# Kernel tuning notes

Measured on AMD Instinct MI355X. Metric: run time of the kernel, lower is better.

## Reference

```python
import jax, jax.numpy as jnp
import numpy as np

RADIUS = 0.1
NSAMPLE = 32


def setup_inputs() -> dict:
    key = jax.random.key(0)
    k1, k2, k3, k4, k5 = jax.random.split(key, 5)
    B, NPOINT, N, C = 4, 2048, 8192, 64
    query_xyz = jax.random.uniform(k1, (B, 3, NPOINT), dtype=jnp.float32)
    support_xyz = jax.random.uniform(k2, (B, 3, N), dtype=jnp.float32)
    query_mask = jax.random.bernoulli(k3, 0.9, (B, NPOINT))
    support_mask = jax.random.bernoulli(k4, 0.9, (B, N))
    features = jax.random.normal(k5, (B, C, N), dtype=jnp.float32)
    return {"query_xyz": query_xyz, "support_xyz": support_xyz,
            "query_mask": query_mask, "support_mask": support_mask,
            "features": features}


def _masked_ordered_ball_query(query_xyz, support_xyz, query_mask, support_mask,
                               radius, nsample):
    # query_xyz: (B,3,npoint), support_xyz: (B,3,N)
    q = query_xyz.transpose(0, 2, 1)    # (B, npoint, 3)
    s = support_xyz.transpose(0, 2, 1)  # (B, N, 3)
    N = s.shape[1]
    # squared pairwise distances via |q|^2 + |s|^2 - 2 q.s  -> (B, npoint, N)
    d2 = (jnp.sum(q * q, -1)[:, :, None]
          + jnp.sum(s * s, -1)[:, None, :]
          - 2.0 * jnp.einsum('bpd,bnd->bpn', q, s))
    within = (d2 <= radius * radius) \
        & support_mask[:, None, :] & query_mask[:, :, None]
    # ordered selection of the first `nsample` in-ball indices (ascending index)
    score = jnp.where(within, N - jnp.arange(N, dtype=jnp.int32), 0)
    vals, idx = jax.lax.top_k(score, nsample)     # (B, npoint, nsample)
    idx_mask = vals > 0                            # true neighbors
    # pad slots with the first found neighbor (0 if none found)
    first = jnp.where(idx_mask[..., :1], idx[..., :1], 0)
    idx = jnp.where(idx_mask, idx, first)
    return idx, idx_mask


def _group(points_nc, idx):
    # points_nc: (B, N, D), idx: (B, npoint, nsample) -> (B, npoint, nsample, D)
    return jax.vmap(lambda p, i: p[i])(points_nc, idx)


def reference(query_xyz, support_xyz, query_mask, support_mask, features):
    idx, idx_mask = _masked_ordered_ball_query(
        query_xyz, support_xyz, query_mask, support_mask, RADIUS, NSAMPLE)
    s = support_xyz.transpose(0, 2, 1)             # (B, N, 3)
    grouped_xyz = _group(s, idx).transpose(0, 3, 1, 2)   # (B,3,npoint,nsample)
    grouped_xyz = grouped_xyz - query_xyz[:, :, :, None]
    grouped_xyz = grouped_xyz / RADIUS             # normalize_xyz=True
    f = features.transpose(0, 2, 1)                # (B, N, C)
    grouped_features = _group(f, idx).transpose(0, 3, 1, 2)  # (B,C,npoint,nsample)
    new_features = jnp.concatenate([grouped_xyz, grouped_features], axis=1)
    return new_features, idx_mask
```

## Files before the change

### kernel.cpp

```cpp
#include <hip/hip_runtime.h>


#define NPOINT 2048
#define NSUP   8192
#define NCH    64
#define NS     32
#define GRID1  10
#define CELLS  1000
#define QCHUNK 1024

__device__ __forceinline__ bool probe_mask4(const void* mask) {
    const unsigned char* mb = (const unsigned char*)mask;
    const int lane = threadIdx.x & 63;
    return __ballot(mb[4 * lane + 1] != 0) == 0ull;
}
__device__ __forceinline__ bool read_mask(const void* mask, int i, bool is4) {
    return is4 ? (((const int*)mask)[i] != 0)
               : (((const unsigned char*)mask)[i] != 0);
}
__device__ __forceinline__ int cell_of(float x, float y, float z) {
    const int cx = min(GRID1 - 1, (int)(x * 10.0f));
    const int cy = min(GRID1 - 1, (int)(y * 10.0f));
    const int cz = min(GRID1 - 1, (int)(z * 10.0f));
    return cx + GRID1 * cy + GRID1 * GRID1 * cz;
}

__global__ __launch_bounds__(256) void zero_ws(int* __restrict__ ptr, int n) {
    const int i = blockIdx.x * 256 + threadIdx.x;
    if (i < n) ptr[i] = 0;
}

__global__ __launch_bounds__(256) void grid_hist(
    const float* __restrict__ support_xyz, const void* __restrict__ support_mask,
    int* __restrict__ starts)
{
    const bool m4 = probe_mask4(support_mask);
    const int gid = blockIdx.x * 256 + threadIdx.x;
    const int b = gid / NSUP, n = gid % NSUP;
    if (!read_mask(support_mask, gid, m4)) return;
    const float* sx = support_xyz + (size_t)b * 3 * NSUP;
    const int cid = cell_of(sx[n], sx[NSUP + n], sx[2 * NSUP + n]);
    atomicAdd(&starts[b * (CELLS + 1) + cid + 1], 1);
}

__global__ __launch_bounds__(1024) void grid_scan(int* __restrict__ starts) {
    __shared__ int scanb[1024];
    const int tid = threadIdx.x;
    int* sb = starts + blockIdx.x * (CELLS + 1);
    scanb[tid] = (tid < CELLS) ? sb[tid + 1] : 0;
    __syncthreads();
    for (int d = 1; d < 1024; d <<= 1) {
        int v = 0;
        if (tid >= d) v = scanb[tid - d];
        __syncthreads();
        if (tid >= d) scanb[tid] += v;
        __syncthreads();
    }
    if (tid < CELLS) sb[tid + 1] = scanb[tid];
}

__global__ __launch_bounds__(256) void grid_fill(
    const float* __restrict__ support_xyz, const void* __restrict__ support_mask,
    const int* __restrict__ starts, int* __restrict__ cursors,
    float4* __restrict__ pts)
{
    const bool m4 = probe_mask4(support_mask);
    const int gid = blockIdx.x * 256 + threadIdx.x;
    const int b = gid / NSUP, n = gid % NSUP;
    if (!read_mask(support_mask, gid, m4)) return;
    const float* sx = support_xyz + (size_t)b * 3 * NSUP;
    const float x = sx[n], y = sx[NSUP + n], z = sx[2 * NSUP + n];
    const int cid = cell_of(x, y, z);
    const int pos = starts[b * (CELLS + 1) + cid]
                  + atomicAdd(&cursors[b * CELLS + cid], 1);
    pts[(size_t)b * NSUP + pos] = make_float4(x, y, z, __int_as_float(n));
}

__global__ __launch_bounds__(256) void mqag_query(
    const float* __restrict__ query_xyz, const float* __restrict__ support_xyz,
    const void* __restrict__ query_mask, const void* __restrict__ support_mask,
    const float4* __restrict__ pts, const int* __restrict__ starts,
    int* __restrict__ idx_ws, float* __restrict__ out, int B)
{
#pragma clang fp contract(off)
    const int wib  = threadIdx.x >> 6;
    const int lane = threadIdx.x & 63;
    const int qid  = blockIdx.x * 4 + wib;
    const int b    = qid / NPOINT;
    const int p    = qid % NPOINT;

    __shared__ int hits_all[4][64];
    __shared__ int slots_all[4][NS];
    int* hits  = hits_all[wib];
    int* slots = slots_all[wib];

    const bool m4s = probe_mask4(support_mask);
    const bool m4q = probe_mask4(query_mask);

    const float* sx = support_xyz + (size_t)b * 3 * NSUP;
    const float* sy = sx + NSUP;
    const float* sz = sx + 2 * NSUP;

    const float qx = query_xyz[(size_t)b * 3 * NPOINT + p];
    const float qy = query_xyz[(size_t)b * 3 * NPOINT + NPOINT + p];
    const float qz = query_xyz[(size_t)b * 3 * NPOINT + 2 * NPOINT + p];
    const bool  qm = read_mask(query_mask, b * NPOINT + p, m4q);
    const float qq = (qx * qx + qy * qy) + qz * qz;

    int cnt = 0;
    if (qm) {
        const int x0 = max(0, (int)floorf((qx - 0.101f) * 10.f));
        const int x1 = min(GRID1 - 1, (int)floorf((qx + 0.101f) * 10.f));
        const int y0 = max(0, (int)floorf((qy - 0.101f) * 10.f));
        const int y1 = min(GRID1 - 1, (int)floorf((qy + 0.101f) * 10.f));
        const int z0 = max(0, (int)floorf((qz - 0.101f) * 10.f));
        const int z1 = min(GRID1 - 1, (int)floorf((qz + 0.101f) * 10.f));
        const int ncx = x1 - x0 + 1;

        const int*    stb  = starts + b * (CELLS + 1);
        const float4* ptsb = pts + (size_t)b * NSUP;

        for (int cz = z0; cz <= z1; ++cz) {
            for (int cy = y0; cy <= y1; ++cy) {
                const int c0 = x0 + GRID1 * cy + GRID1 * GRID1 * cz;
                const int s0 = stb[c0];
                const int e0 = stb[c0 + ncx];
                for (int tb = s0; tb < e0; tb += 64) {
                    const int g  = tb + lane;
                    const bool valid = g < e0;
                    const float4 pv = ptsb[valid ? g : (e0 - 1)];
                    const int nidx = __float_as_int(pv.w);
                    const float ss  = (pv.x * pv.x + pv.y * pv.y) + pv.z * pv.z;
                    const float dot = __builtin_fmaf(qz, pv.z,
                                      __builtin_fmaf(qy, pv.y, qx * pv.x));
                    const float d2  = (qq + ss) - 2.0f * dot;
                    const bool within = valid && (d2 <= 0.01f)
                        && read_mask(support_mask, b * NSUP + nidx, m4s);
                    const unsigned long long bal = __ballot(within);
                    if (within) {
                        const int r = cnt + __popcll(bal & ((1ull << lane) - 1ull));
                        if (r < 64) hits[r] = nidx;
                    }
                    cnt += __popcll(bal);
                }
            }
        }
    }

    __syncthreads();

    if (cnt > 64) {
        int c2 = 0;
        for (int basei = 0; basei < NSUP; basei += 64) {
            const int n = basei + lane;
            const float x = sx[n], y = sy[n], z = sz[n];
            const bool  m = read_mask(support_mask, b * NSUP + n, m4s);
            const float ss  = (x * x + y * y) + z * z;
            const float dot = __builtin_fmaf(qz, z,
                              __builtin_fmaf(qy, y, qx * x));
            const float d2  = (qq + ss) - 2.0f * dot;
            const bool within = (d2 <= 0.01f) && m;
            const unsigned long long bal = __ballot(within);
            if (within) {
                const int r = c2 + __popcll(bal & ((1ull << lane) - 1ull));
                if (r < NS) slots[r] = n;
            }
            c2 += __popcll(bal);
            if (c2 >= NS) break;
        }
        cnt = c2;
    } else {
        int v = (lane < cnt) ? hits[lane] : 0x7FFFFFFF;
        #pragma unroll
        for (int k = 2; k <= 64; k <<= 1) {
            #pragma unroll
            for (int j = k >> 1; j > 0; j >>= 1) {
                const int pv = __shfl_xor(v, j, 64);
                const bool keep_min = ((lane & j) == 0) == ((lane & k) == 0);
                const int mn = min(v, pv), mx = max(v, pv);
                v = keep_min ? mn : mx;
            }
        }
        if (lane < NS && lane < cnt) slots[lane] = v;
    }
    const int found = (cnt < NS) ? cnt : NS;

    __syncthreads();
    const int first = (found > 0) ? slots[0] : 0;
    if (lane < NS && lane >= found) slots[lane] = first;
    __syncthreads();

    if (lane < NS) idx_ws[((size_t)b * NPOINT + p) * NS + lane] = slots[lane];

    const size_t nf_elems = (size_t)B * 67 * NPOINT * NS;
    if (lane < NS) {
        out[nf_elems + ((size_t)b * NPOINT + p) * NS + lane] =
            (lane < found) ? 1.0f : 0.0f;
    }

    for (int i = 0; i < 2; ++i) {
        const int flat = i * 64 + lane;
        if (flat < 3 * NS) {
            const int ch = flat >> 5;
            const int k  = flat & 31;
            const int idx = slots[k];
            const float s = sx[(size_t)ch * NSUP + idx];
            const float q = (ch == 0) ? qx : ((ch == 1) ? qy : qz);
            out[(((size_t)b * 67 + ch) * NPOINT + p) * NS + k] = (s - q) / 0.1f;
        }
    }
}

__global__ __launch_bounds__(256) void gather_feat(
    const float* __restrict__ features, const int* __restrict__ idx_ws,
    float* __restrict__ out, int B)
{
    __shared__ float row[NSUP];
    const int bc = blockIdx.y;
    const int b  = bc / NCH, ch = bc % NCH;
    const int p0 = blockIdx.x * QCHUNK;

    const float* src = features + ((size_t)b * NCH + ch) * NSUP;
    const float4* src4 = (const float4*)src;
    for (int i = threadIdx.x; i < NSUP / 4; i += 256)
        ((float4*)row)[i] = src4[i];
    __syncthreads();

    const int4* idx4 = (const int4*)(idx_ws + ((size_t)b * NPOINT + p0) * NS);
    float4* dst4 = (float4*)(out + (((size_t)b * 67 + 3 + ch) * NPOINT + p0) * NS);
    for (int e = threadIdx.x; e < QCHUNK * NS / 4; e += 256) {
        const int4 iv = idx4[e];
        dst4[e] = make_float4(row[iv.x], row[iv.y], row[iv.z], row[iv.w]);
    }
}

__global__ __launch_bounds__(256) void mqag_linear(
    const float* __restrict__ query_xyz, const float* __restrict__ support_xyz,
    const void* __restrict__ query_mask_raw, const void* __restrict__ support_mask_raw,
    const float* __restrict__ features, float* __restrict__ out, int B)
{
#pragma clang fp contract(off)
    const int wib  = threadIdx.x >> 6;
    const int lane = threadIdx.x & 63;
    const int qid  = blockIdx.x * 4 + wib;
    const int b    = qid / NPOINT;
    const int p    = qid % NPOINT;

    __shared__ int slots_all[4][NS];
    int* slots = slots_all[wib];

    const bool m4s = probe_mask4(support_mask_raw);
    const bool m4q = probe_mask4(query_mask_raw);

    const float* sx = support_xyz + (size_t)b * 3 * NSUP;
    const float* sy = sx + NSUP;
    const float* sz = sx + 2 * NSUP;

    const float qx = query_xyz[(size_t)b * 3 * NPOINT + p];
    const float qy = query_xyz[(size_t)b * 3 * NPOINT + NPOINT + p];
    const float qz = query_xyz[(size_t)b * 3 * NPOINT + 2 * NPOINT + p];
    const bool  qm = read_mask(query_mask_raw, b * NPOINT + p, m4q);
    const float qq = (qx * qx + qy * qy) + qz * qz;

    int cnt = 0;
    if (qm) {
        for (int base = 0; base < NSUP; base += 64) {
            const int n = base + lane;
            const float x = sx[n], y = sy[n], z = sz[n];
            const bool  m = read_mask(support_mask_raw, b * NSUP + n, m4s);
            const float ss  = (x * x + y * y) + z * z;
            const float dot = __builtin_fmaf(qz, z, __builtin_fmaf(qy, y, qx * x));
            const float d2  = (qq + ss) - 2.0f * dot;
            const bool within = (d2 <= 0.01f) && m;
            const unsigned long long bal = __ballot(within);
            if (within) {
                const int r = cnt + __popcll(bal & ((1ull << lane) - 1ull));
                if (r < NS) slots[r] = n;
            }
            cnt += __popcll(bal);
            if (cnt >= NS) break;
        }
    }
    const int found = cnt < NS ? cnt : NS;
    __syncthreads();
    const int first = (found > 0) ? slots[0] : 0;
    if (lane < NS && lane >= found) slots[lane] = first;
    __syncthreads();

    const size_t nf_elems = (size_t)B * 67 * NPOINT * NS;
    if (lane < NS) {
        out[nf_elems + ((size_t)b * NPOINT + p) * NS + lane] =
            (lane < found) ? 1.0f : 0.0f;
    }
    const float* feat = features + (size_t)b * NCH * NSUP;
    for (int i = 0; i < (67 * NS + 63) / 64; ++i) {
        const int flat = i * 64 + lane;
        if (flat < 67 * NS) {
            const int ch = flat >> 5;
            const int k  = flat & 31;
            const int idx = slots[k];
            float val;
            if (ch < 3) {
                const float s = sx[(size_t)ch * NSUP + idx];
                const float q = (ch == 0) ? qx : ((ch == 1) ? qy : qz);
                val = (s - q) / 0.1f;
            } else {
                val = feat[(size_t)(ch - 3) * NSUP + idx];
            }
            out[(((size_t)b * 67 + ch) * NPOINT + p) * NS + k] = val;
        }
    }
}

extern "C" void kernel_launch(void* const* d_in, const int* in_sizes, int n_in,
                              void* d_out, int out_size, void* d_ws, size_t ws_size,
                              hipStream_t stream) {
    const float* query_xyz    = (const float*)d_in[0];
    const float* support_xyz  = (const float*)d_in[1];
    const void*  query_mask   = d_in[2];
    const void*  support_mask = d_in[3];
    const float* features     = (const float*)d_in[4];

    const int B = in_sizes[0] / (3 * NPOINT);

    const size_t off_pts     = 0;
    const size_t off_starts  = off_pts + (size_t)B * NSUP * sizeof(float4);
    const size_t off_cursors = off_starts + (size_t)B * (CELLS + 1) * sizeof(int);
    const size_t off_idx     = off_cursors + (size_t)B * CELLS * sizeof(int);
    const size_t need = off_idx + (size_t)B * NPOINT * NS * sizeof(int);

    if (ws_size >= need) {
        float4* pts  = (float4*)((char*)d_ws + off_pts);
        int* starts  = (int*)((char*)d_ws + off_starts);
        int* cursors = (int*)((char*)d_ws + off_cursors);
        int* idx_ws  = (int*)((char*)d_ws + off_idx);

        const int nzero = B * (CELLS + 1) + B * CELLS;
        hipLaunchKernelGGL(zero_ws, dim3((nzero + 255) / 256), dim3(256), 0,
                           stream, starts, nzero);
        hipLaunchKernelGGL(grid_hist, dim3(B * NSUP / 256), dim3(256), 0,
                           stream, support_xyz, support_mask, starts);
        hipLaunchKernelGGL(grid_scan, dim3(B), dim3(1024), 0, stream, starts);
        hipLaunchKernelGGL(grid_fill, dim3(B * NSUP / 256), dim3(256), 0,
                           stream, support_xyz, support_mask, starts, cursors, pts);
        hipLaunchKernelGGL(mqag_query, dim3(B * NPOINT / 4), dim3(256), 0,
                           stream, query_xyz, support_xyz, query_mask,
                           support_mask, pts, starts, idx_ws, (float*)d_out, B);
        hipLaunchKernelGGL(gather_feat, dim3(NPOINT / QCHUNK, B * NCH), dim3(256),
                           0, stream, features, idx_ws, (float*)d_out, B);
    } else {
        hipLaunchKernelGGL(mqag_linear, dim3(B * NPOINT / 4), dim3(256), 0,
                           stream, query_xyz, support_xyz, query_mask,
                           support_mask, features, (float*)d_out, B);
    }
}
```

Before: 123.3 us.

## Fuse grid build into one per-batch kernel and flatten cell-row scan loop

The four grid-construction kernels (zero, histogram, scan, fill) become a single per-batch block that builds the histogram and cursors in shared memory. This removes three launches and the global atomics. The query kernel now prefix-sums the cell-row lengths across lanes and walks all candidate rows as one flat range, so partially filled 64-wide iterations at each row boundary go away. It also drops the redundant support-mask check, since masked points are never inserted into the grid. In exchange, grid build runs on only B blocks, which leaves most of the device idle and serialises that phase.

New measurement: 116.6 us. 1.06x faster.

```diff
diff --git a/kernel.cpp b/kernel.cpp
--- a/kernel.cpp
+++ b/kernel.cpp
@@ -25,29 +25,35 @@
     return cx + GRID1 * cy + GRID1 * GRID1 * cz;
 }
 
-__global__ __launch_bounds__(256) void zero_ws(int* __restrict__ ptr, int n) {
-    const int i = blockIdx.x * 256 + threadIdx.x;
-    if (i < n) ptr[i] = 0;
-}
-
-__global__ __launch_bounds__(256) void grid_hist(
+__global__ __launch_bounds__(1024) void build_grid(
     const float* __restrict__ support_xyz, const void* __restrict__ support_mask,
-    int* __restrict__ starts)
+    int* __restrict__ starts, float4* __restrict__ pts)
 {
+    __shared__ int hist[CELLS];
+    __shared__ int scanb[1024];
+    __shared__ int cur[CELLS];
+    const int b   = blockIdx.x;
+    const int tid = threadIdx.x;
     const bool m4 = probe_mask4(support_mask);
-    const int gid = blockIdx.x * 256 + threadIdx.x;
-    const int b = gid / NSUP, n = gid % NSUP;
-    if (!read_mask(support_mask, gid, m4)) return;
     const float* sx = support_xyz + (size_t)b * 3 * NSUP;
-    const int cid = cell_of(sx[n], sx[NSUP + n], sx[2 * NSUP + n]);
-    atomicAdd(&starts[b * (CELLS + 1) + cid + 1], 1);
-}
-
-__global__ __launch_bounds__(1024) void grid_scan(int* __restrict__ starts) {
-    __shared__ int scanb[1024];
-    const int tid = threadIdx.x;
-    int* sb = starts + blockIdx.x * (CELLS + 1);
-    scanb[tid] = (tid < CELLS) ? sb[tid + 1] : 0;
+
+    if (tid < CELLS) { hist[tid] = 0; cur[tid] = 0; }
+    __syncthreads();
+
+    float xr[8], yr[8], zr[8]; int cidr[8]; bool mr[8];
+    #pragma unroll
+    for (int i = 0; i < 8; ++i) {
+        const int n = tid + 1024 * i;
+        xr[i] = sx[n];
+        yr[i] = sx[NSUP + n];
+        zr[i] = sx[2 * NSUP + n];
+        mr[i] = read_mask(support_mask, b * NSUP + n, m4);
+        cidr[i] = cell_of(xr[i], yr[i], zr[i]);
+        if (mr[i]) atomicAdd(&hist[cidr[i]], 1);
+    }
+    __syncthreads();
+
+    scanb[tid] = (tid < CELLS) ? hist[tid] : 0;
     __syncthreads();
     for (int d = 1; d < 1024; d <<= 1) {
         int v = 0;
@@ -56,24 +62,20 @@
         if (tid >= d) scanb[tid] += v;
         __syncthreads();
     }
-    if (tid < CELLS) sb[tid + 1] = scanb[tid];
-}
-
-__global__ __launch_bounds__(256) void grid_fill(
-    const float* __restrict__ support_xyz, const void* __restrict__ support_mask,
-    const int* __restrict__ starts, int* __restrict__ cursors,
-    float4* __restrict__ pts)
-{
-    const bool m4 = probe_mask4(support_mask);
-    const int gid = blockIdx.x * 256 + threadIdx.x;
-    const int b = gid / NSUP, n = gid % NSUP;
-    if (!read_mask(support_mask, gid, m4)) return;
-    const float* sx = support_xyz + (size_t)b * 3 * NSUP;
-    const float x = sx[n], y = sx[NSUP + n], z = sx[2 * NSUP + n];
-    const int cid = cell_of(x, y, z);
-    const int pos = starts[b * (CELLS + 1) + cid]
-                  + atomicAdd(&cursors[b * CELLS + cid], 1);
-    pts[(size_t)b * NSUP + pos] = make_float4(x, y, z, __int_as_float(n));
+    int* stg = starts + b * (CELLS + 1);
+    if (tid == 0) stg[0] = 0;
+    if (tid < CELLS) stg[tid + 1] = scanb[tid];
+
+    #pragma unroll
+    for (int i = 0; i < 8; ++i) {
+        if (mr[i]) {
+            const int c    = cidr[i];
+            const int base = (c == 0) ? 0 : scanb[c - 1];
+            const int pos  = base + atomicAdd(&cur[c], 1);
+            pts[(size_t)b * NSUP + pos] =
+                make_float4(xr[i], yr[i], zr[i], __int_as_float(tid + 1024 * i));
+        }
+    }
 }
 
 __global__ __launch_bounds__(256) void mqag_query(
@@ -94,7 +96,6 @@
     int* hits  = hits_all[wib];
     int* slots = slots_all[wib];
 
-    const bool m4s = probe_mask4(support_mask);
     const bool m4q = probe_mask4(query_mask);
 
     const float* sx = support_xyz + (size_t)b * 3 * NSUP;
@@ -107,7 +108,8 @@
     const bool  qm = read_mask(query_mask, b * NPOINT + p, m4q);
     const float qq = (qx * qx + qy * qy) + qz * qz;
 
-    int cnt = 0;
+    int T = 0;
+    int eT[16], aT[16];
     if (qm) {
         const int x0 = max(0, (int)floorf((qx - 0.101f) * 10.f));
         const int x1 = min(GRID1 - 1, (int)floorf((qx + 0.101f) * 10.f));
@@ -116,40 +118,60 @@
         const int z0 = max(0, (int)floorf((qz - 0.101f) * 10.f));
         const int z1 = min(GRID1 - 1, (int)floorf((qz + 0.101f) * 10.f));
         const int ncx = x1 - x0 + 1;
-
-        const int*    stb  = starts + b * (CELLS + 1);
-        const float4* ptsb = pts + (size_t)b * NSUP;
-
-        for (int cz = z0; cz <= z1; ++cz) {
-            for (int cy = y0; cy <= y1; ++cy) {
-                const int c0 = x0 + GRID1 * cy + GRID1 * GRID1 * cz;
-                const int s0 = stb[c0];
-                const int e0 = stb[c0 + ncx];
-                for (int tb = s0; tb < e0; tb += 64) {
-                    const int g  = tb + lane;
-                    const bool valid = g < e0;
-                    const float4 pv = ptsb[valid ? g : (e0 - 1)];
-                    const int nidx = __float_as_int(pv.w);
-                    const float ss  = (pv.x * pv.x + pv.y * pv.y) + pv.z * pv.z;
-                    const float dot = __builtin_fmaf(qz, pv.z,
-                                      __builtin_fmaf(qy, pv.y, qx * pv.x));
-                    const float d2  = (qq + ss) - 2.0f * dot;
-                    const bool within = valid && (d2 <= 0.01f)
-                        && read_mask(support_mask, b * NSUP + nidx, m4s);
-                    const unsigned long long bal = __ballot(within);
-                    if (within) {
-                        const int r = cnt + __popcll(bal & ((1ull << lane) - 1ull));
-                        if (r < 64) hits[r] = nidx;
-                    }
-                    cnt += __popcll(bal);
-                }
-            }
-        }
+        const int* stb = starts + b * (CELLS + 1);
+
+        const int jz = lane >> 2, jy = lane & 3;
+        const int cz = z0 + jz,  cy = y0 + jy;
+        const bool act = (lane < 16) && (cz <= z1) && (cy <= y1);
+        int len = 0, s0 = 0;
+        if (act) {
+            const int c0 = x0 + GRID1 * cy + GRID1 * GRID1 * cz;
+            s0  = stb[c0];
+            len = stb[c0 + ncx] - s0;
+        }
+        int pre = len;
+        #pragma unroll
+        for (int d = 1; d < 64; d <<= 1) {
+            const int v = __shfl_up(pre, d, 64);
+            if (lane >= d) pre += v;
+        }
+        const int adj = s0 - (pre - len);
+        #pragma unroll
+        for (int j = 0; j < 16; ++j) {
+            eT[j] = __builtin_amdgcn_readlane(pre, j);
+            aT[j] = __builtin_amdgcn_readlane(adj, j);
+        }
+        T = eT[15];
+    }
+
+    int cnt = 0;
+    const float4* ptsb = pts + (size_t)b * NSUP;
+    for (int tb = 0; tb < T; tb += 64) {
+        const int  g     = tb + lane;
+        const bool valid = g < T;
+        int adj = 0;
+        #pragma unroll
+        for (int j = 15; j >= 0; --j)
+            if (g < eT[j]) adj = aT[j];
+        const float4 pv = ptsb[valid ? (g + adj) : 0];
+        const int nidx = __float_as_int(pv.w);
+        const float ss  = (pv.x * pv.x + pv.y * pv.y) + pv.z * pv.z;
+        const float dot = __builtin_fmaf(qz, pv.z,
+                          __builtin_fmaf(qy, pv.y, qx * pv.x));
+        const float d2  = (qq + ss) - 2.0f * dot;
+        const bool within = valid && (d2 <= 0.01f);
+        const unsigned long long bal = __ballot(within);
+        if (within) {
+            const int r = cnt + __popcll(bal & ((1ull << lane) - 1ull));
+            if (r < 64) hits[r] = nidx;
+        }
+        cnt += __popcll(bal);
     }
 
     __syncthreads();
 
     if (cnt > 64) {
+        const bool m4s = probe_mask4(support_mask);
         int c2 = 0;
         for (int basei = 0; basei < NSUP; basei += 64) {
             const int n = basei + lane;
@@ -323,26 +345,18 @@
 
     const int B = in_sizes[0] / (3 * NPOINT);
 
-    const size_t off_pts     = 0;
-    const size_t off_starts  = off_pts + (size_t)B * NSUP * sizeof(float4);
-    const size_t off_cursors = off_starts + (size_t)B * (CELLS + 1) * sizeof(int);
-    const size_t off_idx     = off_cursors + (size_t)B * CELLS * sizeof(int);
+    const size_t off_pts    = 0;
+    const size_t off_starts = off_pts + (size_t)B * NSUP * sizeof(float4);
+    const size_t off_idx    = off_starts + (size_t)B * (CELLS + 1) * sizeof(int);
     const size_t need = off_idx + (size_t)B * NPOINT * NS * sizeof(int);
 
     if (ws_size >= need) {
         float4* pts  = (float4*)((char*)d_ws + off_pts);
         int* starts  = (int*)((char*)d_ws + off_starts);
-        int* cursors = (int*)((char*)d_ws + off_cursors);
         int* idx_ws  = (int*)((char*)d_ws + off_idx);
 
-        const int nzero = B * (CELLS + 1) + B * CELLS;
-        hipLaunchKernelGGL(zero_ws, dim3((nzero + 255) / 256), dim3(256), 0,
-                           stream, starts, nzero);
-        hipLaunchKernelGGL(grid_hist, dim3(B * NSUP / 256), dim3(256), 0,
-                           stream, support_xyz, support_mask, starts);
-        hipLaunchKernelGGL(grid_scan, dim3(B), dim3(1024), 0, stream, starts);
-        hipLaunchKernelGGL(grid_fill, dim3(B * NSUP / 256), dim3(256), 0,
-                           stream, support_xyz, support_mask, starts, cursors, pts);
+        hipLaunchKernelGGL(build_grid, dim3(B), dim3(1024), 0, stream,
+                           support_xyz, support_mask, starts, pts);
         hipLaunchKernelGGL(mqag_query, dim3(B * NPOINT / 4), dim3(256), 0,
                            stream, query_xyz, support_xyz, query_mask,
                            support_mask, pts, starts, idx_ws, (float*)d_out, B);
```
